# Kernel optimization log

Hardware: AMD Instinct MI355X
Metric: run time of the kernel (lower is better)

Reference implementation:

```python
import jax, jax.numpy as jnp
import numpy as np

N, D, H, E, K = 65536, 128, 256, 32, 2


def setup_inputs() -> dict:
    key = jax.random.key(0)
    ks = jax.random.split(key, 7)
    s_in = 1.0 / np.sqrt(D)
    s_hid = 1.0 / np.sqrt(H)
    return {
        "x": jax.random.normal(ks[0], (N, D), dtype=jnp.float32),
        "W1": jax.random.uniform(ks[1], (E, D, H), jnp.float32, -s_in, s_in),
        "b1": jax.random.uniform(ks[2], (E, H), jnp.float32, -s_in, s_in),
        "W2": jax.random.uniform(ks[3], (E, H, D), jnp.float32, -s_hid, s_hid),
        "b2": jax.random.uniform(ks[4], (E, D), jnp.float32, -s_hid, s_hid),
        "Wr": jax.random.uniform(ks[5], (D, E), jnp.float32, -s_in, s_in),
        "br": jax.random.uniform(ks[6], (E,), jnp.float32, -s_in, s_in),
    }


def reference(x, W1, b1, W2, b2, Wr, br):
    # Router (eval mode: no gate noise)
    logits = x @ Wr + br                                  # [N, E]
    scores = jax.nn.softmax(logits, axis=-1)              # [N, E]
    topk_vals, topk_inds = jax.lax.top_k(scores, K)       # [N, K]

    # dispatch_mask: zeros scattered with top-k probs (scatter_ on dim 1)
    n = x.shape[0]
    dispatch_mask = jnp.zeros_like(scores).at[
        jnp.arange(n)[:, None], topk_inds
    ].set(topk_vals)                                      # [N, E]

    # Dense all-experts compute, as in the reference torch.stack
    h = jax.nn.relu(jnp.einsum("nd,edh->neh", x, W1) + b1)   # [N, E, H]
    expert_outputs = jnp.einsum("neh,ehd->ned", h, W2) + b2  # [N, E, D]

    output = jnp.einsum("ned,ne->nd", expert_outputs, dispatch_mask)  # [N, D]

    importance = dispatch_mask.sum(axis=0)                # [E]
    imp_mean = jnp.mean(importance)
    imp_var = jnp.var(importance, ddof=1)                 # torch.var is unbiased
    load_balancing_loss = imp_var / (imp_mean ** 2 + 1e-9)
    return output, load_balancing_loss
```

## Files before the change

### kernel.cpp

```cpp
#include <hip/hip_runtime.h>
#include <hip/hip_bf16.h>
#include <cstdint>
#include <cstddef>

#define N_TOK 65536
#define DIM 128
#define HID 256
#define NE 32
#define TOPK 2

typedef __bf16 bf16x8 __attribute__((ext_vector_type(8)));
typedef float f32x4 __attribute__((ext_vector_type(4)));
typedef unsigned uint4v __attribute__((ext_vector_type(4)));

#define LDSA(c, row, byte) ((((c) * 1024 + (row) * 16 + (byte))) ^ ((((c) & 3) << 5)))

__device__ __forceinline__ unsigned short f2bf(float f) {
  unsigned u = __builtin_bit_cast(unsigned, f);
  u += 0x7fffu + ((u >> 16) & 1u);
  return (unsigned short)(u >> 16);
}
__device__ __forceinline__ float bf2f(unsigned s) {
  return __builtin_bit_cast(float, s << 16);
}
__device__ __forceinline__ uint2 split2(float f0, float f1) {
  unsigned u0 = __builtin_bit_cast(unsigned, f0);
  unsigned u1 = __builtin_bit_cast(unsigned, f1);
  unsigned hi = (u0 >> 16) | (u1 & 0xffff0000u);
  float r0 = f0 - __builtin_bit_cast(float, u0 & 0xffff0000u);
  float r1 = f1 - __builtin_bit_cast(float, u1 & 0xffff0000u);
  unsigned lo = (__builtin_bit_cast(unsigned, r0) >> 16) |
                (__builtin_bit_cast(unsigned, r1) & 0xffff0000u);
  uint2 ret; ret.x = hi; ret.y = lo;
  return ret;
}

__global__ void k_zero_out(float* __restrict__ out) {
  int t = blockIdx.x * 256 + threadIdx.x;
  float4 z = make_float4(0.f, 0.f, 0.f, 0.f);
  float4* o4 = (float4*)out;
  o4[t] = z;
  o4[t + 1048576] = z;
}

__global__ __launch_bounds__(256, 3) void k_front(
    const float* __restrict__ x, const float* __restrict__ W1,
    const float* __restrict__ W2, const float* __restrict__ Wr,
    const float* __restrict__ br,
    int* __restrict__ top_idx, float* __restrict__ top_val,
    unsigned short* __restrict__ xb,
    unsigned short* __restrict__ w1t, unsigned short* __restrict__ w2t,
    int* __restrict__ histbuf, float* __restrict__ impbuf) {
  int b = blockIdx.x;
  int t = threadIdx.x;

  if (b >= 1024) {
    int bb = b - 1024;
    const float* in;
    unsigned short* outp;
    int K, r0, c0;
    bool isW1;
    if (bb < 256) {
      int e = bb >> 3, tt = bb & 7;
      in = W1 + (size_t)e * DIM * HID;
      outp = w1t + (size_t)e * DIM * HID;
      K = HID;
      r0 = (tt >> 2) * 64; c0 = (tt & 3) * 64;
      isW1 = true;
    } else {
      bb -= 256;
      int e = bb >> 3, tt = bb & 7;
      in = W2 + (size_t)e * HID * DIM;
      outp = w2t + (size_t)e * HID * DIM;
      K = DIM;
      r0 = (tt >> 1) * 64; c0 = (tt & 1) * 64;
      isW1 = false;
    }
    __shared__ float tile[64][65];
    int r = t >> 2, cs = (t & 3) * 16;
    const float* src = in + (size_t)(r0 + r) * K + c0 + cs;
#pragma unroll
    for (int j = 0; j < 4; ++j) {
      float4 v = *(const float4*)(src + j * 4);
      tile[r][cs + j * 4 + 0] = v.x;
      tile[r][cs + j * 4 + 1] = v.y;
      tile[r][cs + j * 4 + 2] = v.z;
      tile[r][cs + j * 4 + 3] = v.w;
    }
    __syncthreads();
#pragma unroll
    for (int p = 0; p < 2; ++p) {
      int orow = p * 32 + (t >> 3);
      int oc8 = (t & 7) * 8;
      int rr = r0 + oc8;
      unsigned pk[4];
#pragma unroll
      for (int q = 0; q < 4; ++q) {
        unsigned lo = f2bf(tile[oc8 + 2 * q][orow]);
        unsigned hi = f2bf(tile[oc8 + 2 * q + 1][orow]);
        pk[q] = lo | (hi << 16);
      }
      uint4 u;
      u.x = pk[0]; u.y = pk[1]; u.z = pk[2]; u.w = pk[3];
      int h = c0 + orow;
      int hp = isW1 ? ((h & ~63) | ((h & 3) << 4) | ((h & 63) >> 2))
                    : ((h & ~31) | ((h & 1) << 4) | ((h & 31) >> 1));
      size_t addr = (size_t)(rr >> 5) * (K * 32) + (size_t)hp * 32 + (rr & 31);
      *(uint4*)(outp + addr) = u;
    }
    return;
  }

  __shared__ int hc[NE];
  __shared__ float hf[NE];
  __shared__ int slist[64];
  __shared__ int scount;
  if (t < NE) { hc[t] = 0; hf[t] = 0.f; }
  if (t == 0) scount = 0;
  __syncthreads();

  int w = t >> 6, l = t & 63, quad = l >> 4, l15 = l & 15;
  int tok0 = b * 64 + w * 16;

  bf16x8 bfr[2][2][4];
#pragma unroll
  for (int nt = 0; nt < 2; ++nt)
#pragma unroll
    for (int kc = 0; kc < 4; ++kc) {
      unsigned hiw[4], low[4];
#pragma unroll
      for (int jp = 0; jp < 4; ++jp) {
        int k0 = kc * 32 + quad * 8 + jp * 2;
        int e = nt * 16 + l15;
        float w0 = Wr[k0 * NE + e];
        float w1v = Wr[(k0 + 1) * NE + e];
        uint2 s = split2(w0, w1v);
        hiw[jp] = s.x; low[jp] = s.y;
      }
      uint4v h4, l4;
      h4[0] = hiw[0]; h4[1] = hiw[1]; h4[2] = hiw[2]; h4[3] = hiw[3];
      l4[0] = low[0]; l4[1] = low[1]; l4[2] = low[2]; l4[3] = low[3];
      bfr[0][nt][kc] = __builtin_bit_cast(bf16x8, h4);
      bfr[1][nt][kc] = __builtin_bit_cast(bf16x8, l4);
    }

  f32x4 acc[2];
#pragma unroll
  for (int a = 0; a < 2; ++a) {
    f32x4 z = {0.f, 0.f, 0.f, 0.f};
    acc[a] = z;
  }

  {
    const float* xp = x + (size_t)(tok0 + l15) * DIM + quad * 8;
    float4 va[4][2];
#pragma unroll
    for (int kc = 0; kc < 4; ++kc) {
      const float4* p = (const float4*)(xp + kc * 32);
      va[kc][0] = p[0];
      va[kc][1] = p[1];
    }
    unsigned short* xrow = xb + (size_t)(tok0 + l15) * DIM + quad * 8;
#pragma unroll
    for (int kc = 0; kc < 4; ++kc) {
      uint4 u;
      u.x = (unsigned)f2bf(va[kc][0].x) | ((unsigned)f2bf(va[kc][0].y) << 16);
      u.y = (unsigned)f2bf(va[kc][0].z) | ((unsigned)f2bf(va[kc][0].w) << 16);
      u.z = (unsigned)f2bf(va[kc][1].x) | ((unsigned)f2bf(va[kc][1].y) << 16);
      u.w = (unsigned)f2bf(va[kc][1].z) | ((unsigned)f2bf(va[kc][1].w) << 16);
      *(uint4*)(xrow + kc * 32) = u;
    }
#pragma unroll
    for (int kc = 0; kc < 4; ++kc) {
      uint2 s0 = split2(va[kc][0].x, va[kc][0].y);
      uint2 s1 = split2(va[kc][0].z, va[kc][0].w);
      uint2 s2 = split2(va[kc][1].x, va[kc][1].y);
      uint2 s3 = split2(va[kc][1].z, va[kc][1].w);
      uint4v hu, lu;
      hu[0] = s0.x; lu[0] = s0.y;
      hu[1] = s1.x; lu[1] = s1.y;
      hu[2] = s2.x; lu[2] = s2.y;
      hu[3] = s3.x; lu[3] = s3.y;
      bf16x8 ahi = __builtin_bit_cast(bf16x8, hu);
      bf16x8 alo = __builtin_bit_cast(bf16x8, lu);
#pragma unroll
      for (int nt = 0; nt < 2; ++nt) {
        acc[nt] = __builtin_amdgcn_mfma_f32_16x16x32_bf16(ahi, bfr[0][nt][kc], acc[nt], 0, 0, 0);
        acc[nt] = __builtin_amdgcn_mfma_f32_16x16x32_bf16(ahi, bfr[1][nt][kc], acc[nt], 0, 0, 0);
        acc[nt] = __builtin_amdgcn_mfma_f32_16x16x32_bf16(alo, bfr[0][nt][kc], acc[nt], 0, 0, 0);
      }
    }
  }

  float brv0 = br[l15], brv1 = br[16 + l15];
  const float NINF = -3.0e38f;
#pragma unroll
  for (int r = 0; r < 4; ++r) {
    float c0 = acc[0][r] + brv0;
    float c1 = acc[1][r] + brv1;
    float va = (c0 >= c1) ? c0 : c1;
    int ia = (c0 >= c1) ? l15 : 16 + l15;
#pragma unroll
    for (int off = 1; off < 16; off <<= 1) {
      float ov = __shfl_xor(va, off);
      int oi = __shfl_xor(ia, off);
      if (ov > va || (ov == va && oi < ia)) { va = ov; ia = oi; }
    }
    float v1 = va; int i1 = ia;
    float d0 = (i1 == l15) ? NINF : c0;
    float d1 = (i1 == 16 + l15) ? NINF : c1;
    float vb = (d0 >= d1) ? d0 : d1;
    int ib = (d0 >= d1) ? l15 : 16 + l15;
#pragma unroll
    for (int off = 1; off < 16; off <<= 1) {
      float ov = __shfl_xor(vb, off);
      int oi = __shfl_xor(ib, off);
      if (ov > vb || (ov == vb && oi < ib)) { vb = ov; ib = oi; }
    }
    float v2 = vb; int i2 = ib;
    float e0 = (i1 == l15 || i2 == l15) ? NINF : c0;
    float e1 = (i1 == 16 + l15 || i2 == 16 + l15) ? NINF : c1;
    float vc = (e0 >= e1) ? e0 : e1;
#pragma unroll
    for (int off = 1; off < 16; off <<= 1) {
      float ov = __shfl_xor(vc, off);
      vc = (ov > vc) ? ov : vc;
    }
    float s = __expf(c0 - v1) + __expf(c1 - v1);
#pragma unroll
    for (int off = 1; off < 16; off <<= 1) s += __shfl_xor(s, off);
    if (l15 == 0) {
      int n = tok0 + quad * 4 + r;
      int2 ti; ti.x = i1; ti.y = i2;
      float2 tv; tv.x = 1.0f / s; tv.y = __expf(v2 - v1) / s;
      ((int2*)top_idx)[n] = ti;
      ((float2*)top_val)[n] = tv;
      atomicAdd(&hc[i1], 1);
      atomicAdd(&hc[i2], 1);
      atomicAdd(&hf[i1], tv.x);
      atomicAdd(&hf[i2], tv.y);
      if (v2 - vc < 2e-3f) {
        int si = atomicAdd(&scount, 1);
        if (si < 64) slist[si] = n;
      }
    }
  }
  __syncthreads();

  int sc = scount;
  for (int s = (t >> 5); s < sc; s += 8) {
    int lt = t & 31;
    int n = slist[s];
    const float* xr = x + (size_t)n * DIM;
    double a = 0.0;
#pragma unroll 8
    for (int d = 0; d < DIM; ++d) a = fma((double)xr[d], (double)Wr[d * NE + lt], a);
    double lv = a + (double)br[lt];

    double v1 = lv; int i1 = lt;
#pragma unroll
    for (int off = 16; off > 0; off >>= 1) {
      double ov = __shfl_xor(v1, off, 32);
      int oi = __shfl_xor(i1, off, 32);
      if (ov > v1 || (ov == v1 && oi < i1)) { v1 = ov; i1 = oi; }
    }
    double lv2 = (lt == i1) ? -1.0e300 : lv;
    double v2 = lv2; int i2 = lt;
#pragma unroll
    for (int off = 16; off > 0; off >>= 1) {
      double ov = __shfl_xor(v2, off, 32);
      int oi = __shfl_xor(i2, off, 32);
      if (ov > v2 || (ov == v2 && oi < i2)) { v2 = ov; i2 = oi; }
    }
    float p = expf((float)(lv - v1));
    float ssum = p;
#pragma unroll
    for (int off = 16; off > 0; off >>= 1) ssum += __shfl_xor(ssum, off, 32);
    if (lt == 0) {
      int o1 = top_idx[n * 2 + 0];
      int o2 = top_idx[n * 2 + 1];
      float w1v = top_val[n * 2 + 0];
      float w2v = top_val[n * 2 + 1];
      float nv1 = 1.0f / ssum;
      float nv2 = expf((float)(v2 - v1)) / ssum;
      atomicAdd(&hc[o1], -1); atomicAdd(&hc[o2], -1);
      atomicAdd(&hc[i1], 1);  atomicAdd(&hc[i2], 1);
      atomicAdd(&hf[o1], -w1v); atomicAdd(&hf[o2], -w2v);
      atomicAdd(&hf[i1], nv1);  atomicAdd(&hf[i2], nv2);
      top_idx[n * 2 + 0] = i1;
      top_idx[n * 2 + 1] = i2;
      top_val[n * 2 + 0] = nv1;
      top_val[n * 2 + 1] = nv2;
    }
  }
  __syncthreads();
  if (t < NE) {
    histbuf[b * NE + t] = hc[t];
    impbuf[b * NE + t] = hf[t];
  }
}

__global__ __launch_bounds__(256) void k_scatter2(
    const int* __restrict__ top_idx, const float* __restrict__ top_val,
    const int* __restrict__ histbuf, const float* __restrict__ impbuf,
    int* __restrict__ perm, float* __restrict__ gatev, int* __restrict__ inv,
    int* __restrict__ offsets, int* __restrict__ counts, float* __restrict__ out_loss) {
  __shared__ int pf[8][32], pb[8][32];
  __shared__ int offs[NE], pref[NE], h2[NE];
  int b = blockIdx.x, t = threadIdx.x;
  if (t < NE) h2[t] = 0;
  int g = t >> 5, e = t & 31;
  int sf = 0, sb = 0;
  for (int j = 0; j < 128; ++j) {
    int bb = g * 128 + j;
    int v = histbuf[bb * NE + e];
    sf += v;
    sb += (bb < 2 * b) ? v : 0;
  }
  pf[g][e] = sf;
  pb[g][e] = sb;
  __syncthreads();
  if (t < 32) {
    int T = 0, P = 0;
#pragma unroll
    for (int g2 = 0; g2 < 8; ++g2) { T += pf[g2][t]; P += pb[g2][t]; }
    int pc = (T + 63) & ~63;
    int scn = pc;
#pragma unroll
    for (int off = 1; off < 32; off <<= 1) {
      int ov = __shfl_up(scn, off, 32);
      if (t >= off) scn += ov;
    }
    offs[t] = scn - pc;
    pref[t] = P;
    if (b == 0) {
      offsets[t] = scn - pc;
      counts[t] = T;
      if (t == 31) offsets[NE] = scn;
    }
  }
  __syncthreads();
  if (t < 128) {
    int n = b * 128 + t;
    int2 ti = ((const int2*)top_idx)[n];
    float2 tv = ((const float2*)top_val)[n];
    int r0 = atomicAdd(&h2[ti.x], 1);
    int r1 = atomicAdd(&h2[ti.y], 1);
    int p0 = offs[ti.x] + pref[ti.x] + r0;
    int p1 = offs[ti.y] + pref[ti.y] + r1;
    perm[p0] = n;
    gatev[p0] = tv.x;
    perm[p1] = n;
    gatev[p1] = tv.y;
    int2 iv; iv.x = p0; iv.y = p1;
    ((int2*)inv)[n] = iv;
  }
  if (b == 0) {
    __shared__ float pfi[8][32];
    float s2 = 0.f;
    for (int j = 0; j < 128; ++j) s2 += impbuf[(g * 128 + j) * NE + e];
    pfi[g][e] = s2;
    __syncthreads();
    if (t < 32) {
      float imp = 0.f;
#pragma unroll
      for (int g2 = 0; g2 < 8; ++g2) imp += pfi[g2][t];
      float ssum = imp;
#pragma unroll
      for (int off = 16; off > 0; off >>= 1) ssum += __shfl_xor(ssum, off, 32);
      float mean = ssum / 32.0f;
      float dlt = imp - mean;
      float v = dlt * dlt;
#pragma unroll
      for (int off = 16; off > 0; off >>= 1) v += __shfl_xor(v, off, 32);
      if (t == 0) *out_loss = (v / 31.0f) / (mean * mean + 1e-9f);
    }
  }
}

template <int YB>
__global__ __launch_bounds__(256, 3) void k_expert(
    const float* __restrict__ x, const unsigned short* __restrict__ xb,
    const unsigned short* __restrict__ w1t, const unsigned short* __restrict__ w2t,
    const float* __restrict__ b1, const float* __restrict__ b2,
    const int* __restrict__ offsets, const int* __restrict__ counts,
    const int* __restrict__ perm, const float* __restrict__ gatev,
    unsigned short* __restrict__ ybuf, float* __restrict__ out) {
  __shared__ __align__(16) unsigned char smem[32768];

  int bid = (int)(blockIdx.x & 7) * 260 + (int)(blockIdx.x >> 3);
  int slot0 = bid * 64;
  if (slot0 >= offsets[NE]) return;
  int e = 0;
#pragma unroll
  for (int i = 1; i < NE; ++i)
    if (slot0 >= offsets[i]) e = i;
  int cnt = counts[e];
  int local0 = slot0 - offsets[e];
  int nvalid = min(64, cnt - local0);

  int t = threadIdx.x;
  int w = t >> 6;
  int l = t & 63;
  int quad = l >> 4;
  int l15 = l & 15;

  int pvl = 0;
  float gvl = 0.f;
  if (YB) {
    uint4 v[4];
    if (l < nvalid) {
      pvl = perm[slot0 + l];
      gvl = gatev[slot0 + l];
      const uint4* rowp = (const uint4*)(xb + (size_t)pvl * DIM);
#pragma unroll
      for (int cc = 0; cc < 4; ++cc) v[cc] = rowp[w * 4 + cc];
    } else {
#pragma unroll
      for (int cc = 0; cc < 4; ++cc) { v[cc].x = 0u; v[cc].y = 0u; v[cc].z = 0u; v[cc].w = 0u; }
    }
#pragma unroll
    for (int cc = 0; cc < 4; ++cc)
      *(uint4*)(smem + LDSA(w * 4 + cc, l, 0)) = v[cc];
  } else {
    unsigned pk[16];
    if (l < nvalid) {
      pvl = perm[slot0 + l];
      gvl = gatev[slot0 + l];
      const float* src = x + (size_t)pvl * DIM + w * 32;
#pragma unroll
      for (int q = 0; q < 8; ++q) {
        float4 vv = ((const float4*)src)[q];
        pk[q * 2 + 0] = (unsigned)f2bf(vv.x) | ((unsigned)f2bf(vv.y) << 16);
        pk[q * 2 + 1] = (unsigned)f2bf(vv.z) | ((unsigned)f2bf(vv.w) << 16);
      }
    } else {
#pragma unroll
      for (int q = 0; q < 16; ++q) pk[q] = 0u;
    }
#pragma unroll
    for (int cc = 0; cc < 4; ++cc) {
      uint4 u;
      u.x = pk[cc * 4 + 0]; u.y = pk[cc * 4 + 1]; u.z = pk[cc * 4 + 2]; u.w = pk[cc * 4 + 3];
      *(uint4*)(smem + LDSA(w * 4 + cc, l, 0)) = u;
    }
  }

  const unsigned short* w1e = w1t + (size_t)e * DIM * HID;
  bf16x8 w1f[4][4];
#pragma unroll
  for (int kc = 0; kc < 4; ++kc)
#pragma unroll
    for (int jt = 0; jt < 4; ++jt)
      w1f[kc][jt] = *(const bf16x8*)(w1e + kc * 8192 + (w * 64 + jt * 16 + l15) * 32 + quad * 8);

  __syncthreads();

  f32x4 acc[4][4];
#pragma unroll
  for (int a = 0; a < 4; ++a)
#pragma unroll
    for (int bb = 0; bb < 4; ++bb) {
      f32x4 z = {0.f, 0.f, 0.f, 0.f};
      acc[a][bb] = z;
    }
#pragma unroll
  for (int kc = 0; kc < 4; ++kc) {
    bf16x8 af[4];
#pragma unroll
    for (int rt = 0; rt < 4; ++rt)
      af[rt] = *(const bf16x8*)(smem + LDSA(kc * 4 + quad, rt * 16 + l15, 0));
#pragma unroll
    for (int rt = 0; rt < 4; ++rt)
#pragma unroll
      for (int jt = 0; jt < 4; ++jt)
        acc[rt][jt] = __builtin_amdgcn_mfma_f32_16x16x32_bf16(af[rt], w1f[kc][jt], acc[rt][jt], 0, 0, 0);
  }

  const unsigned short* w2e = w2t + (size_t)e * HID * DIM;
  bf16x8 w2f[8][2];
#pragma unroll
  for (int hc = 0; hc < 8; ++hc)
#pragma unroll
    for (int jt = 0; jt < 2; ++jt)
      w2f[hc][jt] = *(const bf16x8*)(w2e + hc * 4096 + (w * 32 + jt * 16 + l15) * 32 + quad * 8);

  __syncthreads();

  {
    float4 b1v = *(const float4*)(b1 + e * HID + w * 64 + 4 * l15);
    int c = w * 8 + (l15 >> 1);
    int byte = (l15 & 1) * 8;
#pragma unroll
    for (int rt = 0; rt < 4; ++rt) {
#pragma unroll
      for (int r = 0; r < 4; ++r) {
        int tokrow = rt * 16 + quad * 4 + r;
        float v0 = acc[rt][0][r] + b1v.x; v0 = v0 > 0.f ? v0 : 0.f;
        float v1 = acc[rt][1][r] + b1v.y; v1 = v1 > 0.f ? v1 : 0.f;
        float v2 = acc[rt][2][r] + b1v.z; v2 = v2 > 0.f ? v2 : 0.f;
        float v3 = acc[rt][3][r] + b1v.w; v3 = v3 > 0.f ? v3 : 0.f;
        uint2 u;
        u.x = (unsigned)f2bf(v0) | ((unsigned)f2bf(v1) << 16);
        u.y = (unsigned)f2bf(v2) | ((unsigned)f2bf(v3) << 16);
        *(uint2*)(smem + LDSA(c, tokrow, byte)) = u;
      }
    }
  }
  __syncthreads();

  f32x4 accc[4][2];
#pragma unroll
  for (int a = 0; a < 4; ++a)
#pragma unroll
    for (int bb = 0; bb < 2; ++bb) {
      f32x4 z = {0.f, 0.f, 0.f, 0.f};
      accc[a][bb] = z;
    }
#pragma unroll
  for (int hc = 0; hc < 8; ++hc) {
    bf16x8 ah[4];
#pragma unroll
    for (int rt = 0; rt < 4; ++rt)
      ah[rt] = *(const bf16x8*)(smem + LDSA(hc * 4 + quad, rt * 16 + l15, 0));
#pragma unroll
    for (int rt = 0; rt < 4; ++rt)
#pragma unroll
      for (int jt = 0; jt < 2; ++jt)
        accc[rt][jt] = __builtin_amdgcn_mfma_f32_16x16x32_bf16(ah[rt], w2f[hc][jt], accc[rt][jt], 0, 0, 0);
  }

  int dbase = w * 32;
  float2 b2v = *(const float2*)(b2 + e * DIM + dbase + 2 * l15);
#pragma unroll
  for (int rt = 0; rt < 4; ++rt) {
#pragma unroll
    for (int r = 0; r < 4; ++r) {
      int tokrow = rt * 16 + quad * 4 + r;
      int pv = __shfl(pvl, tokrow);
      float g = __shfl(gvl, tokrow);
      if (tokrow < nvalid) {
        float y0 = g * (accc[rt][0][r] + b2v.x);
        float y1 = g * (accc[rt][1][r] + b2v.y);
        if (YB) {
          unsigned pack = (unsigned)f2bf(y0) | ((unsigned)f2bf(y1) << 16);
          *(unsigned*)(ybuf + (size_t)(slot0 + tokrow) * DIM + dbase + 2 * l15) = pack;
        } else {
          float* orow = out + (size_t)pv * DIM + dbase + 2 * l15;
          atomicAdd(&orow[0], y0);
          atomicAdd(&orow[1], y1);
        }
      }
    }
  }
}

__global__ __launch_bounds__(256) void k_combine(const unsigned short* __restrict__ ybuf,
                                                 const int* __restrict__ inv,
                                                 float* __restrict__ out) {
  int t = threadIdx.x;
  int n = blockIdx.x * 16 + (t >> 4);
  int lane = t & 15;
  int2 iv = ((const int2*)inv)[n];
  uint4 a = *((const uint4*)(ybuf + (size_t)iv.x * DIM) + lane);
  uint4 b = *((const uint4*)(ybuf + (size_t)iv.y * DIM) + lane);
  unsigned av[4] = {a.x, a.y, a.z, a.w}, bv[4] = {b.x, b.y, b.z, b.w};
  float r[8];
#pragma unroll
  for (int q = 0; q < 4; ++q) {
    r[q * 2 + 0] = bf2f(av[q] & 0xffffu) + bf2f(bv[q] & 0xffffu);
    r[q * 2 + 1] = bf2f(av[q] >> 16) + bf2f(bv[q] >> 16);
  }
  float* orow = out + (size_t)n * DIM + lane * 8;
  float4 w0 = {r[0], r[1], r[2], r[3]}, w1 = {r[4], r[5], r[6], r[7]};
  ((float4*)orow)[0] = w0;
  ((float4*)orow)[1] = w1;
}

extern "C" void kernel_launch(void* const* d_in, const int* in_sizes, int n_in,
                              void* d_out, int out_size, void* d_ws, size_t ws_size,
                              hipStream_t stream) {
  const float* x  = (const float*)d_in[0];
  const float* W1 = (const float*)d_in[1];
  const float* b1 = (const float*)d_in[2];
  const float* W2 = (const float*)d_in[3];
  const float* b2 = (const float*)d_in[4];
  const float* Wr = (const float*)d_in[5];
  const float* br = (const float*)d_in[6];
  float* out = (float*)d_out;

  char* ws = (char*)d_ws;
  int*   counts   = (int*)(ws + 0);
  int*   offsets  = (int*)(ws + 128);
  int*   top_idx  = (int*)(ws + 1024);
  float* top_val  = (float*)(ws + 525312);
  int*   perm     = (int*)(ws + 1049600);
  float* gatev    = (float*)(ws + 1582080);
  int*   inv      = (int*)(ws + 2114560);
  int*   histbuf  = (int*)(ws + 2638848);
  float* impbuf   = (float*)(ws + 2769920);
  unsigned short* w1t = (unsigned short*)(ws + 2900992);
  unsigned short* w2t = (unsigned short*)(ws + 4998144);
  unsigned short* ybuf = (unsigned short*)(ws + 7095296);
  const size_t NEEDED = 41174016;
  bool use_ybuf = ws_size >= NEEDED;

  unsigned short* xb = (unsigned short*)out;

  if (use_ybuf) {
    hipLaunchKernelGGL(k_front, dim3(1536), dim3(256), 0, stream, x, W1, W2, Wr, br,
                       top_idx, top_val, xb, w1t, w2t, histbuf, impbuf);
    hipLaunchKernelGGL(k_scatter2, dim3(512), dim3(256), 0, stream, top_idx, top_val,
                       histbuf, impbuf, perm, gatev, inv, offsets, counts,
                       out + (size_t)N_TOK * DIM);
    hipLaunchKernelGGL((k_expert<1>), dim3(2080), dim3(256), 0, stream, x, xb, w1t, w2t,
                       b1, b2, offsets, counts, perm, gatev, ybuf, out);
    hipLaunchKernelGGL(k_combine, dim3(4096), dim3(256), 0, stream, ybuf, inv, out);
  } else {
    hipLaunchKernelGGL(k_front, dim3(1536), dim3(256), 0, stream, x, W1, W2, Wr, br,
                       top_idx, top_val, xb, w1t, w2t, histbuf, impbuf);
    hipLaunchKernelGGL(k_scatter2, dim3(512), dim3(256), 0, stream, top_idx, top_val,
                       histbuf, impbuf, perm, gatev, inv, offsets, counts,
                       out + (size_t)N_TOK * DIM);
    hipLaunchKernelGGL(k_zero_out, dim3(4096), dim3(256), 0, stream, out);
    hipLaunchKernelGGL((k_expert<0>), dim3(2080), dim3(256), 0, stream, x,
                       (const unsigned short*)0, w1t, w2t, b1, b2, offsets, counts,
                       perm, gatev, (unsigned short*)0, out);
  }
}
```

Before: 179.8 us.

## Fuse scatter, expert and combine into one persistent cooperative kernel

```diff
diff --git a/kernel.cpp b/kernel.cpp
--- a/kernel.cpp
+++ b/kernel.cpp
@@ -1,7 +1,10 @@
 #include <hip/hip_runtime.h>
 #include <hip/hip_bf16.h>
+#include <hip/hip_cooperative_groups.h>
 #include <cstdint>
 #include <cstddef>
+
+namespace cg = cooperative_groups;
 
 #define N_TOK 65536
 #define DIM 128
@@ -300,14 +303,20 @@
   }
 }
 
-__global__ __launch_bounds__(256) void k_scatter2(
+__device__ __forceinline__ void scatter_body(
+    int b, unsigned char* sm,
     const int* __restrict__ top_idx, const float* __restrict__ top_val,
     const int* __restrict__ histbuf, const float* __restrict__ impbuf,
     int* __restrict__ perm, float* __restrict__ gatev, int* __restrict__ inv,
     int* __restrict__ offsets, int* __restrict__ counts, float* __restrict__ out_loss) {
-  __shared__ int pf[8][32], pb[8][32];
-  __shared__ int offs[NE], pref[NE], h2[NE];
-  int b = blockIdx.x, t = threadIdx.x;
+  int (*pf)[32] = (int(*)[32])(sm);
+  int (*pb)[32] = (int(*)[32])(sm + 1024);
+  int* offs = (int*)(sm + 2048);
+  int* pref = (int*)(sm + 2176);
+  int* h2   = (int*)(sm + 2304);
+  float (*pfi)[32] = (float(*)[32])(sm + 2432);
+  int t = threadIdx.x;
+  __syncthreads();
   if (t < NE) h2[t] = 0;
   int g = t >> 5, e = t & 31;
   int sf = 0, sb = 0;
@@ -356,7 +365,6 @@
     ((int2*)inv)[n] = iv;
   }
   if (b == 0) {
-    __shared__ float pfi[8][32];
     float s2 = 0.f;
     for (int j = 0; j < 128; ++j) s2 += impbuf[(g * 128 + j) * NE + e];
     pfi[g][e] = s2;
@@ -379,16 +387,16 @@
 }
 
 template <int YB>
-__global__ __launch_bounds__(256, 3) void k_expert(
+__device__ __forceinline__ void expert_body(
+    int vb, unsigned char* smem,
     const float* __restrict__ x, const unsigned short* __restrict__ xb,
     const unsigned short* __restrict__ w1t, const unsigned short* __restrict__ w2t,
     const float* __restrict__ b1, const float* __restrict__ b2,
     const int* __restrict__ offsets, const int* __restrict__ counts,
     const int* __restrict__ perm, const float* __restrict__ gatev,
     unsigned short* __restrict__ ybuf, float* __restrict__ out) {
-  __shared__ __align__(16) unsigned char smem[32768];
-
-  int bid = (int)(blockIdx.x & 7) * 260 + (int)(blockIdx.x >> 3);
+  __syncthreads();
+  int bid = (vb & 7) * 260 + (vb >> 3);
   int slot0 = bid * 64;
   if (slot0 >= offsets[NE]) return;
   int e = 0;
@@ -555,11 +563,11 @@
   }
 }
 
-__global__ __launch_bounds__(256) void k_combine(const unsigned short* __restrict__ ybuf,
-                                                 const int* __restrict__ inv,
-                                                 float* __restrict__ out) {
+__device__ __forceinline__ void combine_body(int vb, const unsigned short* __restrict__ ybuf,
+                                             const int* __restrict__ inv,
+                                             float* __restrict__ out) {
   int t = threadIdx.x;
-  int n = blockIdx.x * 16 + (t >> 4);
+  int n = vb * 16 + (t >> 4);
   int lane = t & 15;
   int2 iv = ((const int2*)inv)[n];
   uint4 a = *((const uint4*)(ybuf + (size_t)iv.x * DIM) + lane);
@@ -575,6 +583,57 @@
   float4 w0 = {r[0], r[1], r[2], r[3]}, w1 = {r[4], r[5], r[6], r[7]};
   ((float4*)orow)[0] = w0;
   ((float4*)orow)[1] = w1;
+}
+
+__global__ __launch_bounds__(256) void k_scatter2(
+    const int* __restrict__ top_idx, const float* __restrict__ top_val,
+    const int* __restrict__ histbuf, const float* __restrict__ impbuf,
+    int* __restrict__ perm, float* __restrict__ gatev, int* __restrict__ inv,
+    int* __restrict__ offsets, int* __restrict__ counts, float* __restrict__ out_loss) {
+  __shared__ __align__(16) unsigned char sm[3456];
+  scatter_body(blockIdx.x, sm, top_idx, top_val, histbuf, impbuf, perm, gatev, inv,
+               offsets, counts, out_loss);
+}
+
+template <int YB>
+__global__ __launch_bounds__(256, 3) void k_expert(
+    const float* __restrict__ x, const unsigned short* __restrict__ xb,
+    const unsigned short* __restrict__ w1t, const unsigned short* __restrict__ w2t,
+    const float* __restrict__ b1, const float* __restrict__ b2,
+    const int* __restrict__ offsets, const int* __restrict__ counts,
+    const int* __restrict__ perm, const float* __restrict__ gatev,
+    unsigned short* __restrict__ ybuf, float* __restrict__ out) {
+  __shared__ __align__(16) unsigned char smem[32768];
+  expert_body<YB>(blockIdx.x, smem, x, xb, w1t, w2t, b1, b2, offsets, counts, perm,
+                  gatev, ybuf, out);
+}
+
+__global__ __launch_bounds__(256) void k_combine(const unsigned short* __restrict__ ybuf,
+                                                 const int* __restrict__ inv,
+                                                 float* __restrict__ out) {
+  combine_body(blockIdx.x, ybuf, inv, out);
+}
+
+__global__ __launch_bounds__(256, 3) void k_back(
+    const float* x, const unsigned short* xb,
+    const unsigned short* w1t, const unsigned short* w2t,
+    const float* b1, const float* b2,
+    const int* top_idx, const float* top_val,
+    const int* histbuf, const float* impbuf,
+    int* perm, float* gatev, int* inv, int* offsets, int* counts,
+    unsigned short* ybuf, float* out, float* out_loss) {
+  __shared__ __align__(16) unsigned char smem[32768];
+  cg::grid_group grid = cg::this_grid();
+  for (int vb = blockIdx.x; vb < 512; vb += gridDim.x)
+    scatter_body(vb, smem, top_idx, top_val, histbuf, impbuf, perm, gatev, inv,
+                 offsets, counts, out_loss);
+  grid.sync();
+  for (int vb = blockIdx.x; vb < 2080; vb += gridDim.x)
+    expert_body<1>(vb, smem, x, xb, w1t, w2t, b1, b2, offsets, counts, perm,
+                   gatev, ybuf, out);
+  grid.sync();
+  for (int vb = blockIdx.x; vb < 4096; vb += gridDim.x)
+    combine_body(vb, ybuf, inv, out);
 }
 
 extern "C" void kernel_launch(void* const* d_in, const int* in_sizes, int n_in,
@@ -606,22 +665,38 @@
   bool use_ybuf = ws_size >= NEEDED;
 
   unsigned short* xb = (unsigned short*)out;
+  float* out_loss = out + (size_t)N_TOK * DIM;
 
   if (use_ybuf) {
     hipLaunchKernelGGL(k_front, dim3(1536), dim3(256), 0, stream, x, W1, W2, Wr, br,
                        top_idx, top_val, xb, w1t, w2t, histbuf, impbuf);
-    hipLaunchKernelGGL(k_scatter2, dim3(512), dim3(256), 0, stream, top_idx, top_val,
-                       histbuf, impbuf, perm, gatev, inv, offsets, counts,
-                       out + (size_t)N_TOK * DIM);
-    hipLaunchKernelGGL((k_expert<1>), dim3(2080), dim3(256), 0, stream, x, xb, w1t, w2t,
-                       b1, b2, offsets, counts, perm, gatev, ybuf, out);
-    hipLaunchKernelGGL(k_combine, dim3(4096), dim3(256), 0, stream, ybuf, inv, out);
+    int nb = 0;
+    hipError_t oe = hipOccupancyMaxActiveBlocksPerMultiprocessor(&nb, k_back, 256, 0);
+    bool coop_done = false;
+    if (oe == hipSuccess && nb >= 1) {
+      int G = nb * 256;
+      if (G > 2080) G = 2080;
+      void* args[] = {(void*)&x, (void*)&xb, (void*)&w1t, (void*)&w2t, (void*)&b1,
+                      (void*)&b2, (void*)&top_idx, (void*)&top_val, (void*)&histbuf,
+                      (void*)&impbuf, (void*)&perm, (void*)&gatev, (void*)&inv,
+                      (void*)&offsets, (void*)&counts, (void*)&ybuf, (void*)&out,
+                      (void*)&out_loss};
+      hipError_t le = hipLaunchCooperativeKernel((const void*)k_back, dim3(G), dim3(256),
+                                                 args, 0, stream);
+      coop_done = (le == hipSuccess);
+    }
+    if (!coop_done) {
+      hipLaunchKernelGGL(k_scatter2, dim3(512), dim3(256), 0, stream, top_idx, top_val,
+                         histbuf, impbuf, perm, gatev, inv, offsets, counts, out_loss);
+      hipLaunchKernelGGL((k_expert<1>), dim3(2080), dim3(256), 0, stream, x, xb, w1t, w2t,
+                         b1, b2, offsets, counts, perm, gatev, ybuf, out);
+      hipLaunchKernelGGL(k_combine, dim3(4096), dim3(256), 0, stream, ybuf, inv, out);
+    }
   } else {
     hipLaunchKernelGGL(k_front, dim3(1536), dim3(256), 0, stream, x, W1, W2, Wr, br,
                        top_idx, top_val, xb, w1t, w2t, histbuf, impbuf);
     hipLaunchKernelGGL(k_scatter2, dim3(512), dim3(256), 0, stream, top_idx, top_val,
-                       histbuf, impbuf, perm, gatev, inv, offsets, counts,
-                       out + (size_t)N_TOK * DIM);
+                       histbuf, impbuf, perm, gatev, inv, offsets, counts, out_loss);
     hipLaunchKernelGGL(k_zero_out, dim3(4096), dim3(256), 0, stream, out);
     hipLaunchKernelGGL((k_expert<0>), dim3(2080), dim3(256), 0, stream, x,
                        (const unsigned short*)0, w1t, w2t, b1, b2, offsets, counts,
```

Measured after the change: 394.4 us. +119.4%, slower.
